# Performance work log

Hardware: AMD Instinct MI355X
Metric: run time of the kernel (lower is better)

Reference implementation:

```python
import jax, jax.numpy as jnp
import numpy as np

NWIN = 128
HOP = NWIN // 2
BUCKET_FREQS = (32, 32, 64, 64, 64)   # partition of the 256 f-bins (ragged_shapes[-3])
BUCKET_TIMES = (16, 32, 48, 64, 128)  # per-bucket nb_m_bins (ragged_shapes[-1])
EPS = 1e-5


def _bn_relu(x, gamma, beta, axes):
    """Training-mode BatchNorm over `axes` (channel axis = 1) + ReLU, fused."""
    mean = jnp.mean(x, axis=axes, keepdims=True)
    var = jnp.var(x, axis=axes, keepdims=True)  # biased var, as torch BN uses
    bshape = (1, x.shape[1]) + (1,) * (x.ndim - 2)
    g = gamma.reshape(bshape)
    b = beta.reshape(bshape)
    return jax.nn.relu((x - mean) * jax.lax.rsqrt(var + EPS) * g + b)


def setup_inputs() -> dict:
    key = jax.random.key(0)
    ks = jax.random.split(key, 24)
    B, C, F, S = 8, 2, 256, 64
    ncoefs = (S + 1) * HOP  # 4160
    inp = {
        "x": jax.random.normal(ks[0], (B, C, F, ncoefs), jnp.float32),
        "input_mean": jax.random.normal(ks[1], (F,), jnp.float32),
        "input_scale": jax.random.uniform(ks[2], (F,), jnp.float32, 0.5, 1.5),
        "W_deo": jax.random.normal(ks[3], (NWIN, 2 * NWIN), jnp.float32) / np.sqrt(2 * NWIN),
        "gamma_deo": jax.random.uniform(ks[4], (C,), jnp.float32, 0.5, 1.5),
        "beta_deo": 0.1 * jax.random.normal(ks[5], (C,), jnp.float32),
        "nb_slices": S,
    }
    for i, mt in enumerate(BUCKET_TIMES):
        inp[f"W_di{i}"] = jax.random.normal(ks[6 + i], (mt, NWIN), jnp.float32) / np.sqrt(NWIN)
        inp[f"g_di{i}"] = jax.random.uniform(ks[11 + i], (C,), jnp.float32, 0.5, 1.5)
        inp[f"b_di{i}"] = 0.1 * jax.random.normal(ks[16 + i], (C,), jnp.float32)
    return inp


def reference(x, input_mean, input_scale, W_deo, gamma_deo, beta_deo,
              W_di0, W_di1, W_di2, W_di3, W_di4,
              g_di0, g_di1, g_di2, g_di3, g_di4,
              b_di0, b_di1, b_di2, b_di3, b_di4,
              nb_slices):
    # input normalization (permute/add/mul/permute == broadcast over f-bins)
    x = (x + input_mean[:, None]) * input_scale[:, None]  # [B,C,F,T]

    # ---- deoverlap_add: all overlapping windows at once ----
    # torch loop reads slicq[ptr-hop : ptr+nwin+hop] with left pad (slice 0)
    # and right pad (last slice); equivalently pad both ends by HOP and take
    # windows of length 2*NWIN starting at i*HOP.
    x_pad = jnp.pad(x, ((0, 0), (0, 0), (0, 0), (HOP, HOP)))
    win_idx = (jnp.arange(nb_slices)[:, None] * HOP
               + jnp.arange(2 * NWIN)[None, :])          # [S, 2W]
    windows = x_pad[..., win_idx]                        # [B,C,F,S,2W]
    y = jnp.einsum('bcfsw,nw->bcfsn', windows, W_deo)    # [B,C,F,S,W]
    # original applies BN per slice call -> batch stats per (channel, slice)
    y = _bn_relu(y, gamma_deo, beta_deo, axes=(0, 2, 4))

    # ---- deinterpolate: ragged per-bucket Linear + BN3d + ReLU ----
    W_di = (W_di0, W_di1, W_di2, W_di3, W_di4)
    g_di = (g_di0, g_di1, g_di2, g_di3, g_di4)
    b_di = (b_di0, b_di1, b_di2, b_di3, b_di4)
    outs = []
    p = 0
    for freqs, W, g, b in zip(BUCKET_FREQS, W_di, g_di, b_di):
        z = jnp.einsum('bcfst,mt->bcfsm', y[:, :, p:p + freqs], W)
        outs.append(_bn_relu(z, g, b, axes=(0, 2, 3, 4)))
        p += freqs
    return tuple(outs)
```

## Files before the change

kernel.cpp:

```cpp
#include <hip/hip_runtime.h>
#include <cstddef>

#define BB   8
#define CC   2
#define FF   256
#define TT   4160
#define SS   64
#define NW   128
#define KW   256
#define EPSV 1e-5f

typedef __attribute__((ext_vector_type(8))) short bf16x8;
typedef __attribute__((ext_vector_type(4))) float f32x4;

#define YOFF    0
#define ZOFF    16777216
#define W1OFF   25427968
#define W2OFF   25444352
#define STATF   25462784
#define OFF_DA     256
#define OFF_DB     384
#define OFF_DIAB   544
#define OFF_STATR  1024
#define OFF_STATR2 17408
#define NZERO   19456

__device__ __forceinline__ unsigned short f2bf(float f) {
    unsigned int u = __builtin_bit_cast(unsigned int, f);
    u = (u + 0x7FFFu + ((u >> 16) & 1u)) >> 16;
    return (unsigned short)u;
}
__device__ __forceinline__ float bf2f(unsigned short h) {
    return __builtin_bit_cast(float, (unsigned int)h << 16);
}

__global__ __launch_bounds__(256) void k_prep(
    const float* __restrict__ Wdeo,
    const float* __restrict__ Wdi0, const float* __restrict__ Wdi1,
    const float* __restrict__ Wdi2, const float* __restrict__ Wdi3,
    const float* __restrict__ Wdi4,
    unsigned short* __restrict__ w1, unsigned short* __restrict__ w2,
    float* __restrict__ statz)
{
    int gid = blockIdx.x * 256 + threadIdx.x;
    if (gid < NZERO) statz[gid] = 0.f;
    int id = gid - NZERO;
    if (id >= 0 && id < 32768) {
        int j = id & 7, lane = (id >> 3) & 63, nt = (id >> 9) & 7, ks = id >> 12;
        int n = nt * 16 + (lane & 15);
        int k = ks * 32 + ((lane >> 4) << 3) + j;
        w1[id] = f2bf(Wdeo[n * KW + k]);
    }
    id -= 32768;
    if (id >= 0 && id < 36864) {
        const float* W; int base, Tk;
        if (id < 2048)       { W = Wdi0; base = 0;     Tk = 1; }
        else if (id < 6144)  { W = Wdi1; base = 2048;  Tk = 2; }
        else if (id < 12288) { W = Wdi2; base = 6144;  Tk = 3; }
        else if (id < 20480) { W = Wdi3; base = 12288; Tk = 4; }
        else                 { W = Wdi4; base = 20480; Tk = 8; }
        int e = id - base;
        int j = e & 7, lane = (e >> 3) & 63, rest = e >> 9;
        int t = rest % Tk, ks = rest / Tk;
        int n = t * 16 + (lane & 15);
        int k = ks * 32 + ((lane >> 4) << 3) + j;
        w2[id] = f2bf(W[n * NW + k]);
    }
}

__global__ __launch_bounds__(256) void k_deoverlap(
    const float* __restrict__ x, const float* __restrict__ imean,
    const float* __restrict__ iscale, const unsigned short* __restrict__ w1,
    unsigned short* __restrict__ y, float* __restrict__ statR)
{
    __shared__ __align__(16) unsigned short xs[4288];
    __shared__ float psA[4][64], pqA[4][64];
    const int tid = threadIdx.x;
    const int r   = blockIdx.x;
    const int c   = (r >> 8) & 1;

    {
        const float mval = imean[r & 255], sval = iscale[r & 255];
        const float* xr = x + (size_t)r * TT;
        for (int p2 = tid; p2 < 2144; p2 += 256) {
            int i = p2 * 2;
            int t = i - 64;
            float v0 = 0.f, v1 = 0.f;
            if (t >= 0 && t + 1 < TT) {
                float2 xv = *(const float2*)&xr[t];
                v0 = (xv.x + mval) * sval;
                v1 = (xv.y + mval) * sval;
            }
            int phys = i ^ (((i >> 6) & 7) << 3);
            unsigned int pk = (unsigned int)f2bf(v0) | ((unsigned int)f2bf(v1) << 16);
            *(unsigned int*)&xs[phys] = pk;
        }
    }
    __syncthreads();

    const int lane = tid & 63, wv = tid >> 6;
    const int q = lane >> 4, m = lane & 15;

    f32x4 acc[4][2] = {};
    for (int ks = 0; ks < 8; ++ks) {
        const int k0 = ks * 32;
        bf16x8 B0 = *(const bf16x8*)(w1 + ((size_t)((ks * 8 + 2 * wv + 0) * 64 + lane) << 3));
        bf16x8 B1 = *(const bf16x8*)(w1 + ((size_t)((ks * 8 + 2 * wv + 1) * 64 + lane) << 3));
#pragma unroll
        for (int st = 0; st < 4; ++st) {
            int idx  = (st * 16 + m) * 64 + k0 + q * 8;
            int phys = idx ^ (((idx >> 6) & 7) << 3);
            bf16x8 A = *(const bf16x8*)&xs[phys];
            acc[st][0] = __builtin_amdgcn_mfma_f32_16x16x32_bf16(A, B0, acc[st][0], 0, 0, 0);
            acc[st][1] = __builtin_amdgcn_mfma_f32_16x16x32_bf16(A, B1, acc[st][1], 0, 0, 0);
        }
    }

#pragma unroll
    for (int st = 0; st < 4; ++st)
#pragma unroll
        for (int t = 0; t < 2; ++t) {
            int n = (2 * wv + t) * 16 + m;
#pragma unroll
            for (int reg = 0; reg < 4; ++reg) {
                int s = st * 16 + q * 4 + reg;
                y[(size_t)r * 8192 + s * NW + n] = f2bf(acc[st][t][reg]);
            }
        }

#pragma unroll
    for (int st = 0; st < 4; ++st)
#pragma unroll
        for (int reg = 0; reg < 4; ++reg) {
            float ps = 0.f, pq = 0.f;
#pragma unroll
            for (int t = 0; t < 2; ++t) {
                float v = acc[st][t][reg];
                ps += v; pq += v * v;
            }
#pragma unroll
            for (int off = 8; off > 0; off >>= 1) {
                ps += __shfl_down(ps, off, 16);
                pq += __shfl_down(pq, off, 16);
            }
            if (m == 0) {
                int s = st * 16 + q * 4 + reg;
                psA[wv][s] = ps;
                pqA[wv][s] = pq;
            }
        }
    __syncthreads();
    if (tid < 128) {
        int s = tid & 63, which = tid >> 6;
        float v = which ? (pqA[0][s] + pqA[1][s] + pqA[2][s] + pqA[3][s])
                        : (psA[0][s] + psA[1][s] + psA[2][s] + psA[3][s]);
        int rep = blockIdx.x & 63;
        atomicAdd(&statR[rep * 256 + which * 128 + c * SS + s], v);
    }
}

__global__ void k_deo_ab(const float* __restrict__ statR,
                         const float* __restrict__ g, const float* __restrict__ be,
                         float* __restrict__ da, float* __restrict__ db)
{
    int i = threadIdx.x;
    if (i < CC * SS) {
        float sm = 0.f, sq = 0.f;
        for (int rep = 0; rep < 64; ++rep) {
            sm += statR[rep * 256 + i];
            sq += statR[rep * 256 + 128 + i];
        }
        int c = i >> 6;
        const float N = (float)(BB * FF * NW);
        float mean = sm / N;
        float var  = sq / N - mean * mean;
        float a = g[c] * rsqrtf(var + EPSV);
        da[i] = a;
        db[i] = be[c] - mean * a;
    }
}

template <int Tk, int G>
__device__ __forceinline__ void deinterp_body(
    int sub,
    const unsigned short* __restrict__ y, const unsigned short* __restrict__ wb,
    const float* __restrict__ da, const float* __restrict__ db,
    unsigned short* __restrict__ zz, float* __restrict__ statR2,
    int p, int freqs, int kidx, float* ssum, float* ssq)
{
    constexpr int MT = Tk * 16;
    const int tid = threadIdx.x, lane = tid & 63, wv = tid >> 6;
    const int q = lane >> 4, m = lane & 15;
    const int bc = sub & 15;
    const int fg = sub >> 4;
    const int c  = bc & 1;
    const int s  = wv * 16 + m;
    const float aS = da[c * SS + s], bS = db[c * SS + s];

    f32x4 acc[G][Tk] = {};
    const unsigned short* ybase = y + ((size_t)(bc * FF + p + fg * G) * SS) * NW;

#pragma unroll
    for (int ks = 0; ks < 4; ++ks) {
        bf16x8 B[Tk];
#pragma unroll
        for (int t = 0; t < Tk; ++t)
            B[t] = *(const bf16x8*)(wb + ((size_t)((ks * Tk + t) * 64 + lane) << 3));
#pragma unroll
        for (int g = 0; g < G; ++g) {
            bf16x8 ar = *(const bf16x8*)(ybase + ((size_t)g * SS + s) * NW + ks * 32 + q * 8);
            bf16x8 af;
#pragma unroll
            for (int j = 0; j < 8; ++j) {
                float f = bf2f((unsigned short)ar[j]);
                f = fmaxf(fmaf(f, aS, bS), 0.f);
                af[j] = (short)f2bf(f);
            }
#pragma unroll
            for (int t = 0; t < Tk; ++t)
                acc[g][t] = __builtin_amdgcn_mfma_f32_16x16x32_bf16(af, B[t], acc[g][t], 0, 0, 0);
        }
    }

    float ls = 0.f, lq = 0.f;
#pragma unroll
    for (int g = 0; g < G; ++g) {
        size_t zrow = (size_t)(bc * freqs + fg * G + g) * SS;
#pragma unroll
        for (int t = 0; t < Tk; ++t)
#pragma unroll
            for (int reg = 0; reg < 4; ++reg) {
                float v = acc[g][t][reg];
                ls += v; lq += v * v;
                int srow = wv * 16 + q * 4 + reg;
                zz[(zrow + srow) * MT + t * 16 + m] = f2bf(v);
            }
    }
#pragma unroll
    for (int o = 32; o > 0; o >>= 1) {
        ls += __shfl_down(ls, o, 64);
        lq += __shfl_down(lq, o, 64);
    }
    if (lane == 0) { ssum[wv] = ls; ssq[wv] = lq; }
    __syncthreads();
    if (tid == 0) {
        int rep = sub & 63;
        atomicAdd(&statR2[rep * 32 + kidx * 2 + c],      ssum[0] + ssum[1] + ssum[2] + ssum[3]);
        atomicAdd(&statR2[rep * 32 + 16 + kidx * 2 + c], ssq[0] + ssq[1] + ssq[2] + ssq[3]);
    }
}

__global__ __launch_bounds__(256) void k_deinterp_all(
    const unsigned short* __restrict__ y, const unsigned short* __restrict__ w2,
    const float* __restrict__ da, const float* __restrict__ db,
    unsigned short* __restrict__ z, float* __restrict__ statR2)
{
    __shared__ float ssum[4], ssq[4];
    const int b = blockIdx.x;
    if (b < 256) {
        deinterp_body<4, 4>(b,        y, w2 + 12288, da, db, z + 4718592, statR2, 128, 64, 3, ssum, ssq);
    } else if (b < 512) {
        deinterp_body<3, 4>(b - 256,  y, w2 + 6144,  da, db, z + 1572864, statR2,  64, 64, 2, ssum, ssq);
    } else if (b < 1024) {
        deinterp_body<8, 2>(b - 512,  y, w2 + 20480, da, db, z + 8912896, statR2, 192, 64, 4, ssum, ssq);
    } else if (b < 1152) {
        deinterp_body<2, 4>(b - 1024, y, w2 + 2048,  da, db, z + 524288,  statR2,  32, 32, 1, ssum, ssq);
    } else {
        deinterp_body<1, 4>(b - 1152, y, w2 + 0,     da, db, z + 0,       statR2,   0, 32, 0, ssum, ssq);
    }
}

__global__ void k_di_ab(const float* __restrict__ statR2,
                        const float* __restrict__ g0, const float* __restrict__ g1,
                        const float* __restrict__ g2, const float* __restrict__ g3,
                        const float* __restrict__ g4,
                        const float* __restrict__ b0, const float* __restrict__ b1,
                        const float* __restrict__ b2, const float* __restrict__ b3,
                        const float* __restrict__ b4,
                        float* __restrict__ ab)
{
    int i = threadIdx.x;
    if (i < 10) {
        float sm = 0.f, sq = 0.f;
        for (int rep = 0; rep < 64; ++rep) {
            sm += statR2[rep * 32 + i];
            sq += statR2[rep * 32 + 16 + i];
        }
        int kb = i >> 1, c = i & 1;
        const float Nv[5] = {262144.f, 524288.f, 1572864.f, 2097152.f, 4194304.f};
        const float* gp[5] = {g0, g1, g2, g3, g4};
        const float* bp[5] = {b0, b1, b2, b3, b4};
        float mean = sm / Nv[kb];
        float var  = sq / Nv[kb] - mean * mean;
        float a = gp[kb][c] * rsqrtf(var + EPSV);
        ab[i * 2]     = a;
        ab[i * 2 + 1] = bp[kb][c] - mean * a;
    }
}

__global__ __launch_bounds__(256) void k_bn_out(
    const unsigned short* __restrict__ z, const float* __restrict__ ab,
    float* __restrict__ out)
{
    int i4 = blockIdx.x * 256 + threadIdx.x;
    if (i4 >= 4325376) return;
    int kb, off4, cs4;
    if (i4 < 131072)       { kb = 0; off4 = 0;       cs4 = 8192;   }
    else if (i4 < 393216)  { kb = 1; off4 = 131072;  cs4 = 16384;  }
    else if (i4 < 1179648) { kb = 2; off4 = 393216;  cs4 = 49152;  }
    else if (i4 < 2228224) { kb = 3; off4 = 1179648; cs4 = 65536;  }
    else                   { kb = 4; off4 = 2228224; cs4 = 131072; }
    int c = ((i4 - off4) / cs4) & 1;
    float a = ab[(kb * 2 + c) * 2], b = ab[(kb * 2 + c) * 2 + 1];
    ushort4 u = *(const ushort4*)(z + (size_t)i4 * 4);
    float4 o;
    o.x = fmaxf(fmaf(bf2f(u.x), a, b), 0.f);
    o.y = fmaxf(fmaf(bf2f(u.y), a, b), 0.f);
    o.z = fmaxf(fmaf(bf2f(u.z), a, b), 0.f);
    o.w = fmaxf(fmaf(bf2f(u.w), a, b), 0.f);
    *(float4*)(out + (size_t)i4 * 4) = o;
}

extern "C" void kernel_launch(void* const* d_in, const int* in_sizes, int n_in,
                              void* d_out, int out_size, void* d_ws, size_t ws_size,
                              hipStream_t stream)
{
    const float* x      = (const float*)d_in[0];
    const float* imean  = (const float*)d_in[1];
    const float* iscale = (const float*)d_in[2];
    const float* Wdeo   = (const float*)d_in[3];
    const float* gdeo   = (const float*)d_in[4];
    const float* bdeo   = (const float*)d_in[5];
    const float* Wdi[5] = {(const float*)d_in[7],  (const float*)d_in[10],
                           (const float*)d_in[13], (const float*)d_in[16],
                           (const float*)d_in[19]};
    const float* gdi[5] = {(const float*)d_in[8],  (const float*)d_in[11],
                           (const float*)d_in[14], (const float*)d_in[17],
                           (const float*)d_in[20]};
    const float* bdi[5] = {(const float*)d_in[9],  (const float*)d_in[12],
                           (const float*)d_in[15], (const float*)d_in[18],
                           (const float*)d_in[21]};
    float* out = (float*)d_out;
    float* ws  = (float*)d_ws;

    unsigned short* y  = (unsigned short*)(ws + YOFF);
    unsigned short* z  = (unsigned short*)(ws + ZOFF);
    unsigned short* w1 = (unsigned short*)(ws + W1OFF);
    unsigned short* w2 = (unsigned short*)(ws + W2OFF);
    float* st     = ws + STATF;
    float* da     = st + OFF_DA;
    float* db     = st + OFF_DB;
    float* diab   = st + OFF_DIAB;
    float* statR  = st + OFF_STATR;
    float* statR2 = st + OFF_STATR2;

    k_prep<<<348, 256, 0, stream>>>(Wdeo, Wdi[0], Wdi[1], Wdi[2], Wdi[3], Wdi[4],
                                    w1, w2, st);

    k_deoverlap<<<BB * CC * FF, 256, 0, stream>>>(x, imean, iscale, w1, y, statR);
    k_deo_ab<<<1, 128, 0, stream>>>(statR, gdeo, bdeo, da, db);

    k_deinterp_all<<<1280, 256, 0, stream>>>(y, w2, da, db, z, statR2);

    k_di_ab<<<1, 16, 0, stream>>>(statR2,
                                  gdi[0], gdi[1], gdi[2], gdi[3], gdi[4],
                                  bdi[0], bdi[1], bdi[2], bdi[3], bdi[4], diab);

    k_bn_out<<<16896, 256, 0, stream>>>(z, diab, out);
}
```

Measured before the change: 249.9 us.

## Swap MFMA operands for vectorized stores, prefetch weights, parallelize stat reductions

```diff
diff --git a/kernel.cpp b/kernel.cpp
--- a/kernel.cpp
+++ b/kernel.cpp
@@ -102,53 +102,48 @@
     const int q = lane >> 4, m = lane & 15;
 
     f32x4 acc[4][2] = {};
+    bf16x8 Bc0 = *(const bf16x8*)(w1 + ((size_t)((0 * 8 + 2 * wv + 0) * 64 + lane) << 3));
+    bf16x8 Bc1 = *(const bf16x8*)(w1 + ((size_t)((0 * 8 + 2 * wv + 1) * 64 + lane) << 3));
+#pragma unroll
     for (int ks = 0; ks < 8; ++ks) {
+        bf16x8 Bn0, Bn1;
+        if (ks < 7) {
+            Bn0 = *(const bf16x8*)(w1 + ((size_t)(((ks + 1) * 8 + 2 * wv + 0) * 64 + lane) << 3));
+            Bn1 = *(const bf16x8*)(w1 + ((size_t)(((ks + 1) * 8 + 2 * wv + 1) * 64 + lane) << 3));
+        }
         const int k0 = ks * 32;
-        bf16x8 B0 = *(const bf16x8*)(w1 + ((size_t)((ks * 8 + 2 * wv + 0) * 64 + lane) << 3));
-        bf16x8 B1 = *(const bf16x8*)(w1 + ((size_t)((ks * 8 + 2 * wv + 1) * 64 + lane) << 3));
 #pragma unroll
         for (int st = 0; st < 4; ++st) {
             int idx  = (st * 16 + m) * 64 + k0 + q * 8;
             int phys = idx ^ (((idx >> 6) & 7) << 3);
             bf16x8 A = *(const bf16x8*)&xs[phys];
-            acc[st][0] = __builtin_amdgcn_mfma_f32_16x16x32_bf16(A, B0, acc[st][0], 0, 0, 0);
-            acc[st][1] = __builtin_amdgcn_mfma_f32_16x16x32_bf16(A, B1, acc[st][1], 0, 0, 0);
-        }
-    }
-
-#pragma unroll
-    for (int st = 0; st < 4; ++st)
+            acc[st][0] = __builtin_amdgcn_mfma_f32_16x16x32_bf16(Bc0, A, acc[st][0], 0, 0, 0);
+            acc[st][1] = __builtin_amdgcn_mfma_f32_16x16x32_bf16(Bc1, A, acc[st][1], 0, 0, 0);
+        }
+        Bc0 = Bn0; Bc1 = Bn1;
+    }
+
+#pragma unroll
+    for (int st = 0; st < 4; ++st) {
+        float ps = 0.f, pq = 0.f;
 #pragma unroll
         for (int t = 0; t < 2; ++t) {
-            int n = (2 * wv + t) * 16 + m;
+            ushort4 u;
+            u.x = f2bf(acc[st][t][0]);
+            u.y = f2bf(acc[st][t][1]);
+            u.z = f2bf(acc[st][t][2]);
+            u.w = f2bf(acc[st][t][3]);
+            *(ushort4*)&y[(size_t)r * 8192 + (st * 16 + m) * NW + (2 * wv + t) * 16 + q * 4] = u;
 #pragma unroll
             for (int reg = 0; reg < 4; ++reg) {
-                int s = st * 16 + q * 4 + reg;
-                y[(size_t)r * 8192 + s * NW + n] = f2bf(acc[st][t][reg]);
-            }
-        }
-
-#pragma unroll
-    for (int st = 0; st < 4; ++st)
-#pragma unroll
-        for (int reg = 0; reg < 4; ++reg) {
-            float ps = 0.f, pq = 0.f;
-#pragma unroll
-            for (int t = 0; t < 2; ++t) {
                 float v = acc[st][t][reg];
                 ps += v; pq += v * v;
             }
-#pragma unroll
-            for (int off = 8; off > 0; off >>= 1) {
-                ps += __shfl_down(ps, off, 16);
-                pq += __shfl_down(pq, off, 16);
-            }
-            if (m == 0) {
-                int s = st * 16 + q * 4 + reg;
-                psA[wv][s] = ps;
-                pqA[wv][s] = pq;
-            }
-        }
+        }
+        ps += __shfl_xor(ps, 16, 64);  pq += __shfl_xor(pq, 16, 64);
+        ps += __shfl_xor(ps, 32, 64);  pq += __shfl_xor(pq, 32, 64);
+        if (q == 0) { psA[wv][st * 16 + m] = ps; pqA[wv][st * 16 + m] = pq; }
+    }
     __syncthreads();
     if (tid < 128) {
         int s = tid & 63, which = tid >> 6;
@@ -163,13 +158,19 @@
                          const float* __restrict__ g, const float* __restrict__ be,
                          float* __restrict__ da, float* __restrict__ db)
 {
-    int i = threadIdx.x;
-    if (i < CC * SS) {
-        float sm = 0.f, sq = 0.f;
-        for (int rep = 0; rep < 64; ++rep) {
-            sm += statR[rep * 256 + i];
-            sq += statR[rep * 256 + 128 + i];
-        }
+    __shared__ float red[4][256];
+    int tid = threadIdx.x;
+    int i = tid & 127, h = tid >> 7;
+    float sm = 0.f, sq = 0.f;
+    for (int rep = h; rep < 64; rep += 4) {
+        sm += statR[rep * 256 + i];
+        sq += statR[rep * 256 + 128 + i];
+    }
+    red[h][i] = sm; red[h][128 + i] = sq;
+    __syncthreads();
+    if (h == 0) {
+        sm = red[0][i] + red[1][i] + red[2][i] + red[3][i];
+        sq = red[0][128 + i] + red[1][128 + i] + red[2][128 + i] + red[3][128 + i];
         int c = i >> 6;
         const float N = (float)(BB * FF * NW);
         float mean = sm / N;
@@ -218,23 +219,28 @@
             }
 #pragma unroll
             for (int t = 0; t < Tk; ++t)
-                acc[g][t] = __builtin_amdgcn_mfma_f32_16x16x32_bf16(af, B[t], acc[g][t], 0, 0, 0);
+                acc[g][t] = __builtin_amdgcn_mfma_f32_16x16x32_bf16(B[t], af, acc[g][t], 0, 0, 0);
         }
     }
 
     float ls = 0.f, lq = 0.f;
 #pragma unroll
     for (int g = 0; g < G; ++g) {
-        size_t zrow = (size_t)(bc * freqs + fg * G + g) * SS;
-#pragma unroll
-        for (int t = 0; t < Tk; ++t)
+        size_t zrow = ((size_t)(bc * freqs + fg * G + g) * SS + wv * 16 + m) * MT;
+#pragma unroll
+        for (int t = 0; t < Tk; ++t) {
+            ushort4 u;
+            u.x = f2bf(acc[g][t][0]);
+            u.y = f2bf(acc[g][t][1]);
+            u.z = f2bf(acc[g][t][2]);
+            u.w = f2bf(acc[g][t][3]);
+            *(ushort4*)&zz[zrow + t * 16 + q * 4] = u;
 #pragma unroll
             for (int reg = 0; reg < 4; ++reg) {
                 float v = acc[g][t][reg];
                 ls += v; lq += v * v;
-                int srow = wv * 16 + q * 4 + reg;
-                zz[(zrow + srow) * MT + t * 16 + m] = f2bf(v);
             }
+        }
     }
 #pragma unroll
     for (int o = 32; o > 0; o >>= 1) {
@@ -279,22 +285,30 @@
                         const float* __restrict__ b4,
                         float* __restrict__ ab)
 {
-    int i = threadIdx.x;
+    int tid = threadIdx.x;
+    int i = tid >> 4, j = tid & 15;
     if (i < 10) {
         float sm = 0.f, sq = 0.f;
-        for (int rep = 0; rep < 64; ++rep) {
+        for (int rep = j; rep < 64; rep += 16) {
             sm += statR2[rep * 32 + i];
             sq += statR2[rep * 32 + 16 + i];
         }
-        int kb = i >> 1, c = i & 1;
-        const float Nv[5] = {262144.f, 524288.f, 1572864.f, 2097152.f, 4194304.f};
-        const float* gp[5] = {g0, g1, g2, g3, g4};
-        const float* bp[5] = {b0, b1, b2, b3, b4};
-        float mean = sm / Nv[kb];
-        float var  = sq / Nv[kb] - mean * mean;
-        float a = gp[kb][c] * rsqrtf(var + EPSV);
-        ab[i * 2]     = a;
-        ab[i * 2 + 1] = bp[kb][c] - mean * a;
+#pragma unroll
+        for (int o = 8; o > 0; o >>= 1) {
+            sm += __shfl_down(sm, o, 16);
+            sq += __shfl_down(sq, o, 16);
+        }
+        if (j == 0) {
+            int kb = i >> 1, c = i & 1;
+            const float Nv[5] = {262144.f, 524288.f, 1572864.f, 2097152.f, 4194304.f};
+            const float* gp[5] = {g0, g1, g2, g3, g4};
+            const float* bp[5] = {b0, b1, b2, b3, b4};
+            float mean = sm / Nv[kb];
+            float var  = sq / Nv[kb] - mean * mean;
+            float a = gp[kb][c] * rsqrtf(var + EPSV);
+            ab[i * 2]     = a;
+            ab[i * 2 + 1] = bp[kb][c] - mean * a;
+        }
     }
 }
 
@@ -302,23 +316,31 @@
     const unsigned short* __restrict__ z, const float* __restrict__ ab,
     float* __restrict__ out)
 {
-    int i4 = blockIdx.x * 256 + threadIdx.x;
-    if (i4 >= 4325376) return;
-    int kb, off4, cs4;
-    if (i4 < 131072)       { kb = 0; off4 = 0;       cs4 = 8192;   }
-    else if (i4 < 393216)  { kb = 1; off4 = 131072;  cs4 = 16384;  }
-    else if (i4 < 1179648) { kb = 2; off4 = 393216;  cs4 = 49152;  }
-    else if (i4 < 2228224) { kb = 3; off4 = 1179648; cs4 = 65536;  }
-    else                   { kb = 4; off4 = 2228224; cs4 = 131072; }
-    int c = ((i4 - off4) / cs4) & 1;
+    int i8 = blockIdx.x * 256 + threadIdx.x;
+    if (i8 >= 2162688) return;
+    int kb, off8, cs8;
+    if (i8 < 65536)        { kb = 0; off8 = 0;       cs8 = 4096;  }
+    else if (i8 < 196608)  { kb = 1; off8 = 65536;   cs8 = 8192;  }
+    else if (i8 < 589824)  { kb = 2; off8 = 196608;  cs8 = 24576; }
+    else if (i8 < 1114112) { kb = 3; off8 = 589824;  cs8 = 32768; }
+    else                   { kb = 4; off8 = 1114112; cs8 = 65536; }
+    int c = ((i8 - off8) / cs8) & 1;
     float a = ab[(kb * 2 + c) * 2], b = ab[(kb * 2 + c) * 2 + 1];
-    ushort4 u = *(const ushort4*)(z + (size_t)i4 * 4);
-    float4 o;
-    o.x = fmaxf(fmaf(bf2f(u.x), a, b), 0.f);
-    o.y = fmaxf(fmaf(bf2f(u.y), a, b), 0.f);
-    o.z = fmaxf(fmaf(bf2f(u.z), a, b), 0.f);
-    o.w = fmaxf(fmaf(bf2f(u.w), a, b), 0.f);
-    *(float4*)(out + (size_t)i4 * 4) = o;
+    const unsigned short* zp = z + (size_t)i8 * 8;
+    ushort4 u0 = *(const ushort4*)zp;
+    ushort4 u1 = *(const ushort4*)(zp + 4);
+    float4 o0, o1;
+    o0.x = fmaxf(fmaf(bf2f(u0.x), a, b), 0.f);
+    o0.y = fmaxf(fmaf(bf2f(u0.y), a, b), 0.f);
+    o0.z = fmaxf(fmaf(bf2f(u0.z), a, b), 0.f);
+    o0.w = fmaxf(fmaf(bf2f(u0.w), a, b), 0.f);
+    o1.x = fmaxf(fmaf(bf2f(u1.x), a, b), 0.f);
+    o1.y = fmaxf(fmaf(bf2f(u1.y), a, b), 0.f);
+    o1.z = fmaxf(fmaf(bf2f(u1.z), a, b), 0.f);
+    o1.w = fmaxf(fmaf(bf2f(u1.w), a, b), 0.f);
+    float* op = out + (size_t)i8 * 8;
+    *(float4*)op       = o0;
+    *(float4*)(op + 4) = o1;
 }
 
 extern "C" void kernel_launch(void* const* d_in, const int* in_sizes, int n_in,
@@ -358,13 +380,13 @@
                                     w1, w2, st);
 
     k_deoverlap<<<BB * CC * FF, 256, 0, stream>>>(x, imean, iscale, w1, y, statR);
-    k_deo_ab<<<1, 128, 0, stream>>>(statR, gdeo, bdeo, da, db);
+    k_deo_ab<<<1, 512, 0, stream>>>(statR, gdeo, bdeo, da, db);
 
     k_deinterp_all<<<1280, 256, 0, stream>>>(y, w2, da, db, z, statR2);
 
-    k_di_ab<<<1, 16, 0, stream>>>(statR2,
-                                  gdi[0], gdi[1], gdi[2], gdi[3], gdi[4],
-                                  bdi[0], bdi[1], bdi[2], bdi[3], bdi[4], diab);
-
-    k_bn_out<<<16896, 256, 0, stream>>>(z, diab, out);
-}
+    k_di_ab<<<1, 160, 0, stream>>>(statR2,
+                                   gdi[0], gdi[1], gdi[2], gdi[3], gdi[4],
+                                   bdi[0], bdi[1], bdi[2], bdi[3], bdi[4], diab);
+
+    k_bn_out<<<8448, 256, 0, stream>>>(z, diab, out);
+}
```

Measured after the change: 242.4 us. -3.0%, faster.
